# Performance work log

Hardware: AMD Instinct MI355X
Metric: run time of the kernel (lower is better)

The kernel has to match this reference:

```python
import jax, jax.numpy as jnp
import numpy as np
import math


def _strided_value_mask(L, S, dtype):
    # mask_line[L + d] == 0 when |d| is a power-of-two stride in {2,4,...,<=L};
    # value_mask[i, j] = mask_line[L - i + j], i.e. zero where |j - i| is such a stride.
    diff = jnp.abs(jnp.arange(L)[:, None] - jnp.arange(S)[None, :])  # [L, S]
    vm = jnp.ones((L, S), dtype=dtype)
    stride = 2
    while stride <= L:
        vm = vm * (diff != stride).astype(dtype)
        stride *= 2
    return vm


def setup_inputs() -> dict:
    key = jax.random.key(0)
    k1, k2, k3 = jax.random.split(key, 3)
    B, L, H, E = 4, 2048, 8, 64
    D = 64
    return {
        "queries": jax.random.normal(k1, (B, L, H, E), dtype=jnp.float32),
        "keys": jax.random.normal(k2, (B, L, H, E), dtype=jnp.float32),
        "values": jax.random.normal(k3, (B, L, H, D), dtype=jnp.float32),
    }


def reference(queries, keys, values):
    B, L, H, E = queries.shape
    S = keys.shape[1]
    scale = 1.0 / math.sqrt(E)

    # raw scores [B, H, L, S]
    scores = jnp.einsum("blhe,bshe->bhls", queries, keys)
    # multiplicative strided mask (zeroes scores at power-of-two offsets)
    vm = _strided_value_mask(L, S, scores.dtype)  # [L, S]
    scores = scores * vm
    # causal mask: upper triangle -> -inf (mask_flag=True, attn_mask=None path)
    causal = jnp.triu(jnp.ones((L, S), dtype=bool), k=1)
    scores = jnp.where(causal, -jnp.inf, scores)

    # dropout p=0.0 (eval) -> identity
    A = jax.nn.softmax(scale * scores, axis=-1)
    V = jnp.einsum("bhls,bshd->blhd", A, values)
    return V
```

## Files before the change

kernel.cpp:

```cpp
#include <hip/hip_runtime.h>
#include <hip/hip_bf16.h>
#include <stdint.h>

typedef __attribute__((ext_vector_type(8))) short short8;
typedef __attribute__((ext_vector_type(16))) float f32x16;

namespace {
constexpr int NB = 4, NL = 2048, NH = 8, NE = 64, ND = 64;
constexpr float KS = 0.125f * 1.44269504f;
constexpr int RECSZ32 = 2080;
constexpr int NUNIT   = 160;
constexpr int NCHUNK = 40;
constexpr int RECSZ  = 8320;
constexpr int KSTEP  = 64 * NH * NE;
}

__device__ const unsigned char TBL[160] = {
  15,16,17,18,  19,20,21,22,  23,24,25,26,  27,28,29,30,
  31,95,32,96,  33,97,34,98,  35,99,36,100, 37,101,38,102,
  39,103,40,104, 41,105,42,106, 43,107,44,108, 45,109,46,110,
  47,111,175,48, 112,176,49,113, 177,50,114,178, 51,115,179,52,
  116,180,53,117, 181,54,118,182, 55,119,183,56, 120,184,57,121,
  185,58,122,186, 59,123,187,60, 124,188,61,125, 189,62,126,190,
  63,127,191,255,
  0,94,160,254,  1,93,161,253,  2,92,162,252,  3,91,163,251,
  4,90,164,250,  5,89,165,249,  6,88,166,248,  7,87,167,247,
  8,86,168,246,  9,85,169,245, 10,84,170,244, 11,83,171,243,
  12,82,172,242, 13,81,173,241, 14,80,174,240};

__device__ const unsigned char TG[40] = {
  3,7,7,10,11,11,11,14,14,15,15,15,15,
  6,6,9,9,10,10,12,12,13,13,13,13,14,14,
  2,5,5,8,8,8,9,12,12,
  4,4,1,0};
__device__ const unsigned char TT0[40] = {
  0,0,16,0,0,16,32,0,16,0,16,32,48,
  0,14,0,14,16,30,0,14,0,14,28,42,32,46,
  0,0,12,0,12,24,28,28,40,
  0,10,0,0};
__device__ const unsigned char TT1[40] = {
  16,16,32,16,16,32,48,16,32,16,32,48,64,
  14,28,14,28,30,44,14,28,14,28,42,56,46,60,
  12,12,24,12,24,36,40,40,52,
  10,20,8,4};
__device__ const unsigned char TREC[40] = {
  3,10,11,18,21,22,23,32,33,36,37,38,39,
  8,9,15,16,19,20,24,25,28,29,30,31,34,35,
  2,6,7,12,13,14,17,26,27,
  4,5,1,0};
__device__ const unsigned char CUMD[16] = {0,1,2,3,4,6,8,10,12,15,18,21,24,28,32,36};
__device__ const unsigned char NCHD[16] = {1,1,1,1,2,2,2,2,3,3,3,3,4,4,4,4};

__device__ __forceinline__ ushort bfb(float x) {
  __hip_bfloat16 b(x);
  return __builtin_bit_cast(ushort, b);
}
__device__ __forceinline__ uint32_t pkbf(float lo, float hi) {
  return (uint32_t)bfb(lo) | ((uint32_t)bfb(hi) << 16);
}


__global__ __launch_bounds__(256)
void convfrag(const float* __restrict__ Kg, const float* __restrict__ Vg,
              char* __restrict__ kimg, char* __restrict__ vimg)
{
  const int id = blockIdx.x;
  const int kr = id & 31, bh = id >> 5;
  const int b = bh >> 3, h = bh & 7;
  const int tid = threadIdx.x;

  __shared__ __align__(16) char  kt[64 * 128];
  __shared__ __align__(16) float vt[64 * 64];

  const int key = tid >> 2;
  const int e0  = (tid & 3) * 16;
  {
    const float* kp = Kg + (((size_t)b * NL + kr * 64 + key) * NH + h) * NE + e0;
    float4 a = *(const float4*)kp,       c = *(const float4*)(kp + 4);
    float4 d2 = *(const float4*)(kp + 8), f = *(const float4*)(kp + 12);
    uint4 wA = { pkbf(a.x,a.y), pkbf(a.z,a.w), pkbf(c.x,c.y), pkbf(c.z,c.w) };
    uint4 wB = { pkbf(d2.x,d2.y), pkbf(d2.z,d2.w), pkbf(f.x,f.y), pkbf(f.z,f.w) };
    const int sw = (key & 7) << 4;
    *(uint4*)(kt + key * 128 + ((2 * e0)      ^ sw)) = wA;
    *(uint4*)(kt + key * 128 + ((2 * e0 + 16) ^ sw)) = wB;
  }
  {
    const float* vp = Vg + (((size_t)b * NL + kr * 64 + key) * NH + h) * ND + e0;
    float* dst = vt + key * 64 + e0;
    *(float4*)(dst)      = *(const float4*)(vp);
    *(float4*)(dst + 4)  = *(const float4*)(vp + 4);
    *(float4*)(dst + 8)  = *(const float4*)(vp + 8);
    *(float4*)(dst + 12) = *(const float4*)(vp + 12);
  }
  __syncthreads();

  char* kob = kimg + (size_t)bh * 262144 + (size_t)kr * 2 * 4096;
  char* vob = vimg + (size_t)bh * 262144 + (size_t)kr * 2 * 4096;
  #pragma unroll
  for (int it = 0; it < 2; ++it) {
    int lin = it * 256 + tid;
    int fi = lin >> 6, l = lin & 63;
    int tt = fi >> 2, st = fi & 3;
    int ky = tt * 32 + (l & 31);
    int e  = st * 16 + (l >> 5) * 8;
    uint4 w = *(const uint4*)(kt + ky * 128 + ((2 * e) ^ ((ky & 7) << 4)));
    *(uint4*)(kob + tt * 4096 + st * 1024 + l * 16) = w;
  }
  #pragma unroll
  for (int it = 0; it < 2; ++it) {
    int lin = it * 256 + tid;
    int fi = lin >> 6, l = lin & 63;
    int tt = fi >> 2, f = fi & 3;
    int d  = (f >> 1) * 32 + (l & 31);
    int k0 = tt * 32 + (f & 1) * 16 + (l >> 5) * 8;
    const float* c0 = vt + k0 * 64 + d;
    uint4 w = { pkbf(c0[0],   c0[64]),  pkbf(c0[128], c0[192]),
                pkbf(c0[256], c0[320]), pkbf(c0[384], c0[448]) };
    *(uint4*)(vob + tt * 4096 + f * 1024 + l * 16) = w;
  }
}

__global__ __launch_bounds__(256)
void sattn_frag(const float* __restrict__ Qg, const char* __restrict__ kimg,
                const char* __restrict__ vimg, float* __restrict__ W)
{
  const int id   = blockIdx.x;
  const int bh   = id & 31;
  const int ublk = id >> 5;
  const int b = bh >> 3, h = bh & 7;

  const int tid  = threadIdx.x;
  const int wave = tid >> 6;
  const int lane = tid & 63;
  const int ln31 = lane & 31;
  const int hi   = lane >> 5;

  const int e   = TBL[ublk * 4 + wave];
  const int s   = e & 63, k = e >> 6;
  const int t0u = k * 16;
  const int t1u = (t0u + 16 < s + 1) ? t0u + 16 : s + 1;
  const int G   = s >> 4;
  const int rix = 8 * G * (G + 1) + (s & 15) * (G + 1) + k;
  float* rec = W + ((size_t)bh * NUNIT + rix) * RECSZ32;

  const int q0w = s * 32;
  const int qi  = q0w + ln31;
  const char* kb_img = kimg + (size_t)bh * 262144 + lane * 16;
  const char* vb_img = vimg + (size_t)bh * 262144 + lane * 16;

  short8 qf[4];
  {
    const float* qp = Qg + (((size_t)b * NL + qi) * NH + h) * NE;
    #pragma unroll
    for (int st = 0; st < 4; ++st) {
      const float* qpe = qp + st * 16 + hi * 8;
      union { short8 v; uint32_t u[4]; } f;
      #pragma unroll
      for (int j = 0; j < 4; ++j)
        f.u[j] = pkbf(qpe[2 * j] * KS, qpe[2 * j + 1] * KS);
      qf[st] = f.v;
    }
  }

  f32x16 acc0, acc1;
  #pragma unroll
  for (int i = 0; i < 16; ++i) { acc0[i] = 0.f; acc1[i] = 0.f; }
  float ls = 0.f;

  for (int t = t0u; t < t1u; ++t) {
    const char* kp = kb_img + (size_t)t * 4096;
    const char* vp = vb_img + (size_t)t * 4096;
    short8 a00 = *(const short8*)(vp);
    short8 a01 = *(const short8*)(vp + 1024);
    short8 a10 = *(const short8*)(vp + 2048);
    short8 a11 = *(const short8*)(vp + 3072);
    short8 kf0 = *(const short8*)(kp);
    short8 kf1 = *(const short8*)(kp + 1024);
    short8 kf2 = *(const short8*)(kp + 2048);
    short8 kf3 = *(const short8*)(kp + 3072);

    f32x16 sv;
    #pragma unroll
    for (int i = 0; i < 16; ++i) sv[i] = 0.f;
    sv = __builtin_amdgcn_mfma_f32_32x32x16_bf16(kf0, qf[0], sv, 0, 0, 0);
    sv = __builtin_amdgcn_mfma_f32_32x32x16_bf16(kf1, qf[1], sv, 0, 0, 0);
    sv = __builtin_amdgcn_mfma_f32_32x32x16_bf16(kf2, qf[2], sv, 0, 0, 0);
    sv = __builtin_amdgcn_mfma_f32_32x32x16_bf16(kf3, qf[3], sv, 0, 0, 0);

    const int kv0 = t * 32;
    const int delta = q0w - kv0;
    const int qrelh = (qi - kv0) - 4 * hi;
    float ps0 = 0.f, ps1 = 0.f;
    if (t == s) {
      #pragma unroll
      for (int r = 0; r < 16; ++r) {
        const int cr = (r & 3) + 8 * (r >> 2);
        int diff = qrelh - cr;
        float lg = sv[r];
        bool p2 = (diff > 1) & ((diff & (diff - 1)) == 0);
        lg = p2 ? 0.f : lg;
        lg = (diff < 0) ? -__builtin_inff() : lg;
        float p = exp2f(lg);
        sv[r] = p; (r & 1 ? ps1 : ps0) += p;
      }
    } else {
      int pmax = 1 << (31 - __clz(delta + 31));
      if (pmax >= delta - 31) {
        #pragma unroll
        for (int r = 0; r < 16; ++r) {
          const int cr = (r & 3) + 8 * (r >> 2);
          int diff = qrelh - cr;
          bool p2 = (diff > 1) & ((diff & (diff - 1)) == 0);
          float p = exp2f(p2 ? 0.f : sv[r]);
          sv[r] = p; (r & 1 ? ps1 : ps0) += p;
        }
      } else {
        #pragma unroll
        for (int r = 0; r < 16; ++r) {
          float p = exp2f(sv[r]);
          sv[r] = p; (r & 1 ? ps1 : ps0) += p;
        }
      }
    }
    ls += ps0 + ps1;

    uint32_t w0 = pkbf(sv[0],  sv[1]),  w1 = pkbf(sv[2],  sv[3]);
    uint32_t w2 = pkbf(sv[4],  sv[5]),  w3 = pkbf(sv[6],  sv[7]);
    uint32_t w4 = pkbf(sv[8],  sv[9]),  w5 = pkbf(sv[10], sv[11]);
    uint32_t w6 = pkbf(sv[12], sv[13]), w7 = pkbf(sv[14], sv[15]);
    uint32_t y0 = __shfl_xor(hi ? w0 : w2, 32);
    uint32_t y1 = __shfl_xor(hi ? w1 : w3, 32);
    uint32_t y2 = __shfl_xor(hi ? w4 : w6, 32);
    uint32_t y3 = __shfl_xor(hi ? w5 : w7, 32);
    union { short8 v; uint32_t u[4]; } f0, f1;
    if (hi == 0) {
      f0.u[0] = w0; f0.u[1] = w1; f0.u[2] = y0; f0.u[3] = y1;
      f1.u[0] = w4; f1.u[1] = w5; f1.u[2] = y2; f1.u[3] = y3;
    } else {
      f0.u[0] = y0; f0.u[1] = y1; f0.u[2] = w2; f0.u[3] = w3;
      f1.u[0] = y2; f1.u[1] = y3; f1.u[2] = w6; f1.u[3] = w7;
    }

    acc0 = __builtin_amdgcn_mfma_f32_32x32x16_bf16(a00, f0.v, acc0, 0, 0, 0);
    acc0 = __builtin_amdgcn_mfma_f32_32x32x16_bf16(a01, f1.v, acc0, 0, 0, 0);
    acc1 = __builtin_amdgcn_mfma_f32_32x32x16_bf16(a10, f0.v, acc1, 0, 0, 0);
    acc1 = __builtin_amdgcn_mfma_f32_32x32x16_bf16(a11, f1.v, acc1, 0, 0, 0);
  }

  ls += __shfl_xor(ls, 32);
  #pragma unroll
  for (int r = 0; r < 16; ++r) {
    int d = (r & 3) + 8 * (r >> 2) + 4 * hi;
    rec[d * 32 + ln31]        = acc0[r];
    rec[(32 + d) * 32 + ln31] = acc1[r];
  }
  if (hi == 0) rec[2048 + ln31] = ls;
}

__global__ __launch_bounds__(256)
void sattn_combine32(const float* __restrict__ W, float* __restrict__ Og)
{
  const int id = blockIdx.x;
  const int s  = id & 63, bh = id >> 6;
  const int b = bh >> 3, h = bh & 7;
  const int tid = threadIdx.x;

  const int G = s >> 4, i = s & 15;
  const int cum = 8 * G * (G + 1) + i * (G + 1);
  const int nc  = G + 1;
  const float* rec0 = W + ((size_t)bh * NUNIT + cum) * RECSZ32;

  __shared__ float sd[64][33];
  __shared__ float Lq[32];

  {
    int d = tid >> 2, q4 = (tid & 3) * 8;
    float4 a0 = {0,0,0,0}, a1 = {0,0,0,0};
    for (int c = 0; c < nc; ++c) {
      const float* rp = rec0 + (size_t)c * RECSZ32 + d * 32 + q4;
      float4 v0 = *(const float4*)rp, v1 = *(const float4*)(rp + 4);
      a0.x += v0.x; a0.y += v0.y; a0.z += v0.z; a0.w += v0.w;
      a1.x += v1.x; a1.y += v1.y; a1.z += v1.z; a1.w += v1.w;
    }
    sd[d][q4+0] = a0.x; sd[d][q4+1] = a0.y; sd[d][q4+2] = a0.z; sd[d][q4+3] = a0.w;
    sd[d][q4+4] = a1.x; sd[d][q4+5] = a1.y; sd[d][q4+6] = a1.z; sd[d][q4+7] = a1.w;
  }
  if (tid < 32) {
    float a = 0.f;
    for (int c = 0; c < nc; ++c) a += rec0[(size_t)c * RECSZ32 + 2048 + tid];
    Lq[tid] = 1.0f / a;
  }
  __syncthreads();
  {
    int q = tid >> 3, d8 = (tid & 7) * 8;
    float l = Lq[q];
    float4 o0 = { sd[d8+0][q]*l, sd[d8+1][q]*l, sd[d8+2][q]*l, sd[d8+3][q]*l };
    float4 o1 = { sd[d8+4][q]*l, sd[d8+5][q]*l, sd[d8+6][q]*l, sd[d8+7][q]*l };
    float* op = Og + (((size_t)b * NL + s * 32 + q) * NH + h) * ND + d8;
    *(float4*)op = o0; *(float4*)(op + 4) = o1;
  }
}

#define LD(RR) do {                                                         \
    const float* kp_ = kpp + (size_t)(RR) * KSTEP;                          \
    const float* vp_ = vpp + (size_t)(RR) * KSTEP;                          \
    kx0 = *(const float4*)(kp_);      kx1 = *(const float4*)(kp_ + 4);      \
    kx2 = *(const float4*)(kp_ + 8);  kx3 = *(const float4*)(kp_ + 12);     \
    vx0 = *(const float4*)(vp_);               vx1 = *(const float4*)(vp_ + NH*ND); \
    vx2 = *(const float4*)(vp_ + 2*NH*ND);     vx3 = *(const float4*)(vp_ + 3*NH*ND); \
  } while (0)

#define STG(KB, VB) do {                                                    \
    uint4 kwA = { pkbf(kx0.x,kx0.y), pkbf(kx0.z,kx0.w),                     \
                  pkbf(kx1.x,kx1.y), pkbf(kx1.z,kx1.w) };                   \
    uint4 kwB = { pkbf(kx2.x,kx2.y), pkbf(kx2.z,kx2.w),                     \
                  pkbf(kx3.x,kx3.y), pkbf(kx3.z,kx3.w) };                   \
    *(uint4*)((KB) + krow*128 + ( kcol2        ^ kswz)) = kwA;              \
    *(uint4*)((KB) + krow*128 + ((kcol2 + 16)  ^ kswz)) = kwB;              \
    _Pragma("unroll")                                                       \
    for (int j_ = 0; j_ < 4; ++j_) {                                        \
      int d_ = vd0 + j_;                                                    \
      char* vr_ = (VB) + d_*128;                                            \
      int vs_ = (d_ & 7) << 4;                                              \
      *(uint32_t*)(vr_ + ((vk0*2    ) ^ vs_)) = pkbf(vx0[j_], vx1[j_]);     \
      *(uint32_t*)(vr_ + ((vk0*2 + 4) ^ vs_)) = pkbf(vx2[j_], vx3[j_]);     \
    }                                                                       \
  } while (0)

#define COMPUTE(TT, SUB, KB, VB) do {                                       \
    const int kv0_ = (TT) * 32;                                             \
    f32x16 s;                                                               \
    _Pragma("unroll")                                                       \
    for (int i_ = 0; i_ < 16; ++i_) s[i_] = 0.f;                            \
    { const char* kb_ = (const char*)(KB) + ((SUB)*32 + ln31) * 128;        \
      _Pragma("unroll")                                                     \
      for (int st_ = 0; st_ < 4; ++st_) {                                   \
        short8 kf_ = *(const short8*)(kb_ + ((st_*32 + hi*16) ^ rsw));      \
        s = __builtin_amdgcn_mfma_f32_32x32x16_bf16(kf_, qf[st_], s, 0,0,0);\
      } }                                                                   \
    const int delta_ = q0w - kv0_;                                          \
    const int qrelh_ = (qi - kv0_) - 4 * hi;                                \
    if ((TT) == tw) {                                                       \
      _Pragma("unroll")                                                     \
      for (int r_ = 0; r_ < 16; ++r_) {                                     \
        const int cr_ = (r_ & 3) + 8 * (r_ >> 2);                           \
        int diff_ = qrelh_ - cr_;                                           \
        float lg_ = s[r_];                                                  \
        bool p2_ = (diff_ > 1) & ((diff_ & (diff_ - 1)) == 0);              \
        lg_ = p2_ ? 0.f : lg_;                                              \
        lg_ = (diff_ < 0) ? -__builtin_inff() : lg_;                        \
        s[r_] = exp2f(lg_);                                                 \
      }                                                                     \
    } else {                                                                \
      int pmax_ = 1 << (31 - __clz(delta_ + 31));                           \
      if (pmax_ >= delta_ - 31) {                                           \
        _Pragma("unroll")                                                   \
        for (int r_ = 0; r_ < 16; ++r_) {                                   \
          const int cr_ = (r_ & 3) + 8 * (r_ >> 2);                         \
          int diff_ = qrelh_ - cr_;                                         \
          bool p2_ = (diff_ > 1) & ((diff_ & (diff_ - 1)) == 0);            \
          s[r_] = exp2f(p2_ ? 0.f : s[r_]);                                 \
        }                                                                   \
      } else {                                                              \
        _Pragma("unroll")                                                   \
        for (int r_ = 0; r_ < 16; ++r_) s[r_] = exp2f(s[r_]);               \
      }                                                                     \
    }                                                                       \
    uint32_t w0_ = pkbf(s[0],  s[1]),  w1_ = pkbf(s[2],  s[3]);             \
    uint32_t w2_ = pkbf(s[4],  s[5]),  w3_ = pkbf(s[6],  s[7]);             \
    uint32_t w4_ = pkbf(s[8],  s[9]),  w5_ = pkbf(s[10], s[11]);            \
    uint32_t w6_ = pkbf(s[12], s[13]), w7_ = pkbf(s[14], s[15]);            \
    uint32_t y0_ = __shfl_xor(hi ? w0_ : w2_, 32);                          \
    uint32_t y1_ = __shfl_xor(hi ? w1_ : w3_, 32);                          \
    uint32_t y2_ = __shfl_xor(hi ? w4_ : w6_, 32);                          \
    uint32_t y3_ = __shfl_xor(hi ? w5_ : w7_, 32);                          \
    union { short8 v; uint32_t u[4]; } f0_, f1_;                            \
    if (hi == 0) {                                                          \
      f0_.u[0] = w0_; f0_.u[1] = w1_; f0_.u[2] = y0_; f0_.u[3] = y1_;       \
      f1_.u[0] = w4_; f1_.u[1] = w5_; f1_.u[2] = y2_; f1_.u[3] = y3_;       \
    } else {                                                                \
      f0_.u[0] = y0_; f0_.u[1] = y1_; f0_.u[2] = w2_; f0_.u[3] = w3_;       \
      f1_.u[0] = y2_; f1_.u[1] = y3_; f1_.u[2] = w6_; f1_.u[3] = w7_;       \
    }                                                                       \
    { const char* vr0_ = (const char*)(VB) + ln31 * 128;                    \
      const char* vr1_ = (const char*)(VB) + (32 + ln31) * 128;             \
      short8 a00_ = *(const short8*)(vr0_ + (((SUB)*64      + hi*16) ^ rsw));\
      short8 a01_ = *(const short8*)(vr0_ + (((SUB)*64 + 32 + hi*16) ^ rsw));\
      short8 a10_ = *(const short8*)(vr1_ + (((SUB)*64      + hi*16) ^ rsw));\
      short8 a11_ = *(const short8*)(vr1_ + (((SUB)*64 + 32 + hi*16) ^ rsw));\
      acc0 = __builtin_amdgcn_mfma_f32_32x32x16_bf16(a00_, f0_.v, acc0, 0,0,0); \
      acc0 = __builtin_amdgcn_mfma_f32_32x32x16_bf16(a01_, f1_.v, acc0, 0,0,0); \
      acc1 = __builtin_amdgcn_mfma_f32_32x32x16_bf16(a10_, f0_.v, acc1, 0,0,0); \
      acc1 = __builtin_amdgcn_mfma_f32_32x32x16_bf16(a11_, f1_.v, acc1, 0,0,0); \
      accl = __builtin_amdgcn_mfma_f32_32x32x16_bf16(onesv, f0_.v, accl, 0,0,0);\
      accl = __builtin_amdgcn_mfma_f32_32x32x16_bf16(onesv, f1_.v, accl, 0,0,0);\
    }                                                                       \
  } while (0)

__global__ __launch_bounds__(256, 3)
void sattn_mid(const float* __restrict__ Qg, const float* __restrict__ Kg,
               const float* __restrict__ Vg, float* __restrict__ W)
{
  const int id = blockIdx.x;
  const int bh = id & 31;
  const int e  = id >> 5;
  const int g  = TG[e];
  const int t0 = TT0[e], t1 = TT1[e];
  float* rec = W + (size_t)(bh * NCHUNK + TREC[e]) * RECSZ;
  const int b = bh >> 3, h = bh & 7;

  const int tid  = threadIdx.x;
  const int wave = tid >> 6;
  const int lane = tid & 63;
  const int ln31 = lane & 31;
  const int hi   = lane >> 5;

  __shared__ __align__(16) struct { ushort kt[64 * 64]; ushort vt[64 * 64]; } lds;

  const int q0w = g * 128 + wave * 32;
  const int qi  = q0w + ln31;
  const int tw  = 4 * g + wave;
  const int rsw = (ln31 & 7) << 4;

  short8 qf[4];
  {
    const float* qp = Qg + (((size_t)b * NL + qi) * NH + h) * NE;
    #pragma unroll
    for (int st = 0; st < 4; ++st) {
      const float* qpe = qp + st * 16 + hi * 8;
      union { short8 v; uint32_t u[4]; } f;
      #pragma unroll
      for (int j = 0; j < 4; ++j)
        f.u[j] = pkbf(qpe[2 * j] * KS, qpe[2 * j + 1] * KS);
      qf[st] = f.v;
    }
  }
  short8 onesv;
  {
    union { short8 v; uint32_t u[4]; } o;
    #pragma unroll
    for (int j = 0; j < 4; ++j) o.u[j] = 0x3F803F80u;
    onesv = o.v;
  }

  f32x16 acc0, acc1, accl;
  #pragma unroll
  for (int i = 0; i < 16; ++i) { acc0[i] = 0.f; acc1[i] = 0.f; accl[i] = 0.f; }

  const int krow = tid >> 2,        kcol = (tid & 3) * 16;
  const int vk0  = (tid & 15) * 4,  vd0  = (tid >> 4) * 4;
  const int kbase = t0 * 32;
  const float* kpp = Kg + (((size_t)b * NL + kbase + krow) * NH + h) * NE + kcol;
  const float* vpp = Vg + (((size_t)b * NL + kbase + vk0 ) * NH + h) * ND + vd0;
  const int kswz  = (krow & 7) << 4;
  const int kcol2 = kcol * 2;

  float4 kx0, kx1, kx2, kx3, vx0, vx1, vx2, vx3;

  const int nr = (t1 - t0) >> 1;
  LD(0);
  STG((char*)lds.kt, (char*)lds.vt);
  __syncthreads();
  if (nr > 1) LD(1);
  for (int r = 0;;) {
    const int tt = t0 + 2 * r;
    if (tt     <= tw) COMPUTE(tt,     0, (char*)lds.kt, (char*)lds.vt);
    if (tt + 1 <= tw) COMPUTE(tt + 1, 1, (char*)lds.kt, (char*)lds.vt);
    if (++r == nr) break;
    __syncthreads();
    STG((char*)lds.kt, (char*)lds.vt);
    __syncthreads();
    if (r + 1 < nr) LD(r + 1);
  }

  #pragma unroll
  for (int r = 0; r < 16; ++r) {
    int d = (r & 3) + 8 * (r >> 2) + 4 * hi;
    rec[d * 128 + wave * 32 + ln31]        = acc0[r];
    rec[(32 + d) * 128 + wave * 32 + ln31] = acc1[r];
  }
  if (hi == 0) rec[8192 + wave * 32 + ln31] = accl[0];
}

__global__ __launch_bounds__(256)
void sattn_combine(const float* __restrict__ W, float* __restrict__ Og)
{
  const int id = blockIdx.x;
  const int h2 = id & 1, g = (id >> 1) & 15, bh = id >> 5;
  const int b = bh >> 3, h = bh & 7;
  const int tid = threadIdx.x;

  __shared__ float sd[64][67];
  __shared__ float Lq[64];

  const float* rec0 = W + (size_t)(bh * NCHUNK + CUMD[g]) * RECSZ;
  const int nc = NCHD[g];

  #pragma unroll
  for (int rep = 0; rep < 4; ++rep) {
    int d  = rep * 16 + (tid >> 4);
    int q4 = (tid & 15) * 4;
    float4 a = {0.f, 0.f, 0.f, 0.f};
    for (int c = 0; c < nc; ++c) {
      float4 v = *(const float4*)(rec0 + (size_t)c * RECSZ + d * 128 + h2 * 64 + q4);
      a.x += v.x; a.y += v.y; a.z += v.z; a.w += v.w;
    }
    sd[d][q4 + 0] = a.x; sd[d][q4 + 1] = a.y;
    sd[d][q4 + 2] = a.z; sd[d][q4 + 3] = a.w;
  }
  if (tid < 64) {
    float a = 0.f;
    for (int c = 0; c < nc; ++c) a += rec0[(size_t)c * RECSZ + 8192 + h2 * 64 + tid];
    Lq[tid] = 1.0f / a;
  }
  __syncthreads();
  #pragma unroll
  for (int rep = 0; rep < 4; ++rep) {
    int q  = rep * 16 + (tid >> 4);
    int d4 = (tid & 15) * 4;
    float l = Lq[q];
    float4 o = { sd[d4][q] * l, sd[d4 + 1][q] * l, sd[d4 + 2][q] * l, sd[d4 + 3][q] * l };
    *(float4*)(Og + (((size_t)b * NL + g * 128 + h2 * 64 + q) * NH + h) * ND + d4) = o;
  }
}

extern "C" void kernel_launch(void* const* d_in, const int* in_sizes, int n_in,
                              void* d_out, int out_size, void* d_ws, size_t ws_size,
                              hipStream_t stream) {
  const float* Q = (const float*)d_in[0];
  const float* K = (const float*)d_in[1];
  const float* V = (const float*)d_in[2];
  float* O = (float*)d_out;
  const size_t recbytes = (size_t)32 * NUNIT * RECSZ32 * sizeof(float);
  const size_t imgsz    = (size_t)32 * 64 * 4096;
  const size_t need_full = recbytes + 2 * imgsz;
  float* W = (float*)d_ws;
  if (ws_size >= need_full) {
    char* kimg = (char*)d_ws + recbytes;
    char* vimg = kimg + imgsz;
    convfrag       <<<dim3(1024), dim3(256), 0, stream>>>(K, V, kimg, vimg);
    sattn_frag     <<<dim3(1280), dim3(256), 0, stream>>>(Q, kimg, vimg, W);
    sattn_combine32<<<dim3(2048), dim3(256), 0, stream>>>(W, O);
  } else {
    sattn_mid      <<<dim3(32 * NCHUNK), dim3(256), 0, stream>>>(Q, K, V, W);
    sattn_combine  <<<dim3(1024), dim3(256), 0, stream>>>(W, O);
  }
}
```

Before: 70.60 us.

## Split frag kernel into 2-wave blocks, reorder units, compute row sums via MFMA

The attention-fragment kernel now launches twice as many 128-thread blocks with two waves each, and uses a new ordering table that schedules the heaviest work units first (longest-processing-time style) for better load balance. The per-tile softmax denominator, previously a scalar accumulation with a cross-lane shuffle, is now computed by two extra MFMA instructions against a ones vector. This removes the VALU adds at the cost of extra matrix work, and the sum is now accumulated from bf16-rounded probabilities rather than fp32 values. An unused need_mid size is also added.

New measurement: 66.93 us. 1.05x faster.

```diff
diff --git a/kernel.cpp b/kernel.cpp
--- a/kernel.cpp
+++ b/kernel.cpp
@@ -15,18 +15,20 @@
 constexpr int KSTEP  = 64 * NH * NE;
 }
 
-__device__ const unsigned char TBL[160] = {
-  15,16,17,18,  19,20,21,22,  23,24,25,26,  27,28,29,30,
-  31,95,32,96,  33,97,34,98,  35,99,36,100, 37,101,38,102,
-  39,103,40,104, 41,105,42,106, 43,107,44,108, 45,109,46,110,
-  47,111,175,48, 112,176,49,113, 177,50,114,178, 51,115,179,52,
-  116,180,53,117, 181,54,118,182, 55,119,183,56, 120,184,57,121,
-  185,58,122,186, 59,123,187,60, 124,188,61,125, 189,62,126,190,
+__device__ const unsigned char ORD[160] = {
   63,127,191,255,
-  0,94,160,254,  1,93,161,253,  2,92,162,252,  3,91,163,251,
-  4,90,164,250,  5,89,165,249,  6,88,166,248,  7,87,167,247,
-  8,86,168,246,  9,85,169,245, 10,84,170,244, 11,83,171,243,
-  12,82,172,242, 13,81,173,241, 14,80,174,240};
+  48,112,176, 49,113,177, 50,114,178, 51,115,179, 52,116,180,
+  53,117,181, 54,118,182, 55,119,183, 56,120,184, 57,121,185,
+  58,122,186, 59,123,187, 60,124,188, 61,125,189, 62,126,190,
+  47,111,175,
+  32,96, 33,97, 34,98, 35,99, 36,100, 37,101, 38,102, 39,103,
+  40,104, 41,105, 42,106, 43,107, 44,108, 45,109, 46,110,
+  31,95,
+  15,16,17,18,19,20,21,22,23,24,25,26,27,28,29,30,
+  14,94,174,254, 13,93,173,253, 12,92,172,252, 11,91,171,251,
+  10,90,170,250,  9,89,169,249,  8,88,168,248,  7,87,167,247,
+   6,86,166,246,  5,85,165,245,  4,84,164,244,  3,83,163,243,
+   2,82,162,242,  1,81,161,241,  0,80,160,240};
 
 __device__ const unsigned char TG[40] = {
   3,7,7,10,11,11,11,14,14,15,15,15,15,
@@ -120,13 +122,13 @@
   }
 }
 
-__global__ __launch_bounds__(256)
+__global__ __launch_bounds__(128)
 void sattn_frag(const float* __restrict__ Qg, const char* __restrict__ kimg,
                 const char* __restrict__ vimg, float* __restrict__ W)
 {
   const int id   = blockIdx.x;
   const int bh   = id & 31;
-  const int ublk = id >> 5;
+  const int pair = id >> 5;
   const int b = bh >> 3, h = bh & 7;
 
   const int tid  = threadIdx.x;
@@ -135,7 +137,7 @@
   const int ln31 = lane & 31;
   const int hi   = lane >> 5;
 
-  const int e   = TBL[ublk * 4 + wave];
+  const int e   = ORD[pair * 2 + wave];
   const int s   = e & 63, k = e >> 6;
   const int t0u = k * 16;
   const int t1u = (t0u + 16 < s + 1) ? t0u + 16 : s + 1;
@@ -161,11 +163,17 @@
       qf[st] = f.v;
     }
   }
-
-  f32x16 acc0, acc1;
-  #pragma unroll
-  for (int i = 0; i < 16; ++i) { acc0[i] = 0.f; acc1[i] = 0.f; }
-  float ls = 0.f;
+  short8 onesv;
+  {
+    union { short8 v; uint32_t u[4]; } o;
+    #pragma unroll
+    for (int j = 0; j < 4; ++j) o.u[j] = 0x3F803F80u;
+    onesv = o.v;
+  }
+
+  f32x16 acc0, acc1, accl;
+  #pragma unroll
+  for (int i = 0; i < 16; ++i) { acc0[i] = 0.f; acc1[i] = 0.f; accl[i] = 0.f; }
 
   for (int t = t0u; t < t1u; ++t) {
     const char* kp = kb_img + (size_t)t * 4096;
@@ -190,7 +198,6 @@
     const int kv0 = t * 32;
     const int delta = q0w - kv0;
     const int qrelh = (qi - kv0) - 4 * hi;
-    float ps0 = 0.f, ps1 = 0.f;
     if (t == s) {
       #pragma unroll
       for (int r = 0; r < 16; ++r) {
@@ -200,8 +207,7 @@
         bool p2 = (diff > 1) & ((diff & (diff - 1)) == 0);
         lg = p2 ? 0.f : lg;
         lg = (diff < 0) ? -__builtin_inff() : lg;
-        float p = exp2f(lg);
-        sv[r] = p; (r & 1 ? ps1 : ps0) += p;
+        sv[r] = exp2f(lg);
       }
     } else {
       int pmax = 1 << (31 - __clz(delta + 31));
@@ -211,18 +217,13 @@
           const int cr = (r & 3) + 8 * (r >> 2);
           int diff = qrelh - cr;
           bool p2 = (diff > 1) & ((diff & (diff - 1)) == 0);
-          float p = exp2f(p2 ? 0.f : sv[r]);
-          sv[r] = p; (r & 1 ? ps1 : ps0) += p;
+          sv[r] = exp2f(p2 ? 0.f : sv[r]);
         }
       } else {
         #pragma unroll
-        for (int r = 0; r < 16; ++r) {
-          float p = exp2f(sv[r]);
-          sv[r] = p; (r & 1 ? ps1 : ps0) += p;
-        }
+        for (int r = 0; r < 16; ++r) sv[r] = exp2f(sv[r]);
       }
     }
-    ls += ps0 + ps1;
 
     uint32_t w0 = pkbf(sv[0],  sv[1]),  w1 = pkbf(sv[2],  sv[3]);
     uint32_t w2 = pkbf(sv[4],  sv[5]),  w3 = pkbf(sv[6],  sv[7]);
@@ -245,16 +246,17 @@
     acc0 = __builtin_amdgcn_mfma_f32_32x32x16_bf16(a01, f1.v, acc0, 0, 0, 0);
     acc1 = __builtin_amdgcn_mfma_f32_32x32x16_bf16(a10, f0.v, acc1, 0, 0, 0);
     acc1 = __builtin_amdgcn_mfma_f32_32x32x16_bf16(a11, f1.v, acc1, 0, 0, 0);
-  }
-
-  ls += __shfl_xor(ls, 32);
+    accl = __builtin_amdgcn_mfma_f32_32x32x16_bf16(onesv, f0.v, accl, 0, 0, 0);
+    accl = __builtin_amdgcn_mfma_f32_32x32x16_bf16(onesv, f1.v, accl, 0, 0, 0);
+  }
+
   #pragma unroll
   for (int r = 0; r < 16; ++r) {
     int d = (r & 3) + 8 * (r >> 2) + 4 * hi;
     rec[d * 32 + ln31]        = acc0[r];
     rec[(32 + d) * 32 + ln31] = acc1[r];
   }
-  if (hi == 0) rec[2048 + ln31] = ls;
+  if (hi == 0) rec[2048 + ln31] = accl[0];
 }
 
 __global__ __launch_bounds__(256)
@@ -534,12 +536,13 @@
   const size_t recbytes = (size_t)32 * NUNIT * RECSZ32 * sizeof(float);
   const size_t imgsz    = (size_t)32 * 64 * 4096;
   const size_t need_full = recbytes + 2 * imgsz;
+  const size_t need_mid  = (size_t)32 * NCHUNK * RECSZ * sizeof(float);
   float* W = (float*)d_ws;
   if (ws_size >= need_full) {
     char* kimg = (char*)d_ws + recbytes;
     char* vimg = kimg + imgsz;
     convfrag       <<<dim3(1024), dim3(256), 0, stream>>>(K, V, kimg, vimg);
-    sattn_frag     <<<dim3(1280), dim3(256), 0, stream>>>(Q, kimg, vimg, W);
+    sattn_frag     <<<dim3(2560), dim3(128), 0, stream>>>(Q, kimg, vimg, W);
     sattn_combine32<<<dim3(2048), dim3(256), 0, stream>>>(W, O);
   } else {
     sattn_mid      <<<dim3(32 * NCHUNK), dim3(256), 0, stream>>>(Q, K, V, W);
```
